# Kernel tuning notes

Hardware: AMD Instinct MI355X
Metric: run time of the kernel (lower is better)

The kernel has to match this reference:

```python
import jax, jax.numpy as jnp
import numpy as np

H, HKV, D, HID = 32, 8, 128, 4096
L, CTX, S = 64, 64, 8192
T = CTX + L
HALF = D // 2
EPS = 1e-6
WP = 4096


def setup_inputs() -> dict:
    key = jax.random.key(0)
    ks = jax.random.split(key, 16)
    f = jnp.float32
    w = 0.02
    return {
        "x": jax.random.normal(ks[0], (1, L, HID), f),
        "x_ctx": jax.random.normal(ks[1], (1, CTX, HID), f),
        "cos_q": jax.random.uniform(ks[2], (1, 1, L, HALF), f, -1.0, 1.0),
        "sin_q": jax.random.uniform(ks[3], (1, 1, L, HALF), f, -1.0, 1.0),
        "cos_k": jax.random.uniform(ks[4], (1, 1, T, HALF), f, -1.0, 1.0),
        "sin_k": jax.random.uniform(ks[5], (1, 1, T, HALF), f, -1.0, 1.0),
        "cache_K_in": jax.random.normal(ks[6], (1, HKV, S, D), f),
        "cache_V_in": jax.random.normal(ks[7], (1, HKV, S, D), f),
        "causal_mask": jnp.ones((1, 1, L, WP + T), dtype=bool),
        "Wq": jax.random.normal(ks[8], (HID, H * D), f) * w,
        "Wk": jax.random.normal(ks[9], (HID, HKV * D), f) * w,
        "Wv": jax.random.normal(ks[10], (HID, HKV * D), f) * w,
        "Wo": jax.random.normal(ks[11], (H * D, HID), f) * w,
        "q_norm_w": jnp.ones((D,), f),
        "k_norm_w": jnp.ones((D,), f),
        "write_pos": WP,
        "rotate": 0,
    }


def _rmsnorm(x, w):
    # normalize over head_dim (last axis)
    var = jnp.mean(x * x, axis=-1, keepdims=True)
    return x * jax.lax.rsqrt(var + EPS) * w


def _rope(x, cos, sin):
    # x: (B, H, T, D); cos/sin: (1, 1, T, HALF) -- rotate-half convention
    x1, x2 = x[..., :HALF], x[..., HALF:]
    return jnp.concatenate([x1 * cos - x2 * sin, x2 * cos + x1 * sin], axis=-1)


def reference(x, x_ctx, cos_q, sin_q, cos_k, sin_k, cache_K_in, cache_V_in,
              causal_mask, Wq, Wk, Wv, Wo, q_norm_w, k_norm_w, write_pos, rotate):
    c = jnp.concatenate([x_ctx, x], axis=1)                  # (1, T, HID)
    q = (x @ Wq).reshape(1, L, H, D)
    k = (c @ Wk).reshape(1, T, HKV, D)
    v = (c @ Wv).reshape(1, T, HKV, D)
    q = _rmsnorm(q, q_norm_w).transpose(0, 2, 1, 3)          # (1, H, L, D)
    k = _rmsnorm(k, k_norm_w).transpose(0, 2, 1, 3)          # (1, HKV, T, D)
    v = v.transpose(0, 2, 1, 3)                               # (1, HKV, T, D)
    q = _rope(q, cos_q, sin_q)
    k = _rope(k, cos_k, sin_k)

    if rotate:  # static Python branch (rotate is a compile-time constant)
        attend_K = jnp.concatenate([cache_K_in[:, :, T:S], k], axis=2)
        attend_V = jnp.concatenate([cache_V_in[:, :, T:S], v], axis=2)
    elif write_pos == 0:
        attend_K, attend_V = k, v
    else:
        attend_K = jnp.concatenate([cache_K_in[:, :, :write_pos], k], axis=2)
        attend_V = jnp.concatenate([cache_V_in[:, :, :write_pos], v], axis=2)

    rep = H // HKV
    scale = jnp.float32(D) ** -0.5
    qg = q.reshape(1, HKV, rep, L, D)
    # grouped attention: broadcast KV heads inline instead of materializing expand
    scores = jnp.einsum('bgrld,bgad->bgrla', qg, attend_K) * scale
    scores = jnp.where(causal_mask[:, :, None], scores, -jnp.inf)  # (1,1,1,L,A) bcast
    probs = jax.nn.softmax(scores, axis=-1)
    o = jnp.einsum('bgrla,bgad->bgrld', probs, attend_V)     # (1, HKV, rep, L, D)
    o = o.reshape(1, H, L, D).transpose(0, 2, 1, 3).reshape(1, L, H * D)
    return (o @ Wo, k, v)
```

## Files before the change

kernel.cpp:

```cpp
#include <hip/hip_runtime.h>

typedef unsigned short u16;
typedef __bf16 bf16x8 __attribute__((ext_vector_type(8)));
typedef float f32x4 __attribute__((ext_vector_type(4)));
typedef u16 u16x8 __attribute__((ext_vector_type(8)));

#define NSPLIT 22
#define KSPLIT 4
#define KC 1024
#define NKT 16
#define OSPLIT 8
#define SCALE_Q 0.08838834764831843f

__device__ __forceinline__ u16 f2bf(float f) {
    unsigned u = __builtin_bit_cast(unsigned, f);
    u += 0x7fff + ((u >> 16) & 1);
    return (u16)(u >> 16);
}
__device__ __forceinline__ float bf2f(u16 h) {
    unsigned u = ((unsigned)h) << 16;
    return __builtin_bit_cast(float, u);
}
__device__ __forceinline__ f32x4 mfma16(bf16x8 a, bf16x8 b, f32x4 c) {
    return __builtin_amdgcn_mfma_f32_16x16x32_bf16(a, b, c, 0, 0, 0);
}

__global__ __launch_bounds__(256)
void k_prep(const float* __restrict__ x, const float* __restrict__ xctx,
            u16* __restrict__ fragA)
{
    int tid = blockIdx.x * 256 + threadIdx.x;
    int row = tid >> 9;
    int kc = tid & 511;
    int k0 = kc << 3;
    const float* src = (row < 64) ? (xctx + (size_t)row * 4096)
                                  : (x + (size_t)(row - 64) * 4096);
    f32x4 v0 = *(const f32x4*)&src[k0];
    f32x4 v1 = *(const f32x4*)&src[k0 + 4];
    u16x8 o;
    o[0] = f2bf(v0[0]); o[1] = f2bf(v0[1]); o[2] = f2bf(v0[2]); o[3] = f2bf(v0[3]);
    o[4] = f2bf(v1[0]); o[5] = f2bf(v1[1]); o[6] = f2bf(v1[2]); o[7] = f2bf(v1[3]);
    int ks32 = k0 >> 5;
    int lg = (k0 >> 3) & 3;
    int rt = row >> 4;
    int l = lg * 16 + (row & 15);
    *(u16x8*)&fragA[(((size_t)ks32 * 8 + rt) * 64 + l) * 8] = o;
}

__global__ __launch_bounds__(256)
void k_qkv(const u16* __restrict__ fragA,
           const float* __restrict__ Wq, const float* __restrict__ Wk,
           const float* __restrict__ Wv, float* __restrict__ part)
{
    const int col0 = blockIdx.x * 32;
    const int ksp = blockIdx.y;
    const int ks0 = ksp * KC;
    const float* W; int ldw, cbase, mat;
    if (col0 < 4096)      { W = Wq; ldw = 4096; cbase = col0;        mat = 0; }
    else if (col0 < 5120) { W = Wk; ldw = 1024; cbase = col0 - 4096; mat = 1; }
    else                  { W = Wv; ldw = 1024; cbase = col0 - 5120; mat = 2; }
    const bool full = (mat != 0);
    const int rowbase = full ? 0 : 64;

    __shared__ __align__(16) u16 Bs[32 * 64];

    const int t = threadIdx.x;
    const int w = t >> 6, l = t & 63;
    const int lm = l & 15, lg = l >> 4;

    const int bk = (t >> 3) << 1;
    const int bn4 = (t & 7) << 2;

    f32x4 pb[2];
    f32x4 acc[2][2] = {};

    const int rt0 = full ? (w * 2) : (4 + w);

    #define QKV_BLOAD(kt_)                                                     \
    {                                                                          \
        const int kg = ks0 + (kt_) * 64;                                       \
        pb[0] = *(const f32x4*)&W[(size_t)(kg + bk) * ldw + cbase + bn4];      \
        pb[1] = *(const f32x4*)&W[(size_t)(kg + bk + 1) * ldw + cbase + bn4];  \
    }

    #define QKV_BSTORE()                                                       \
    {                                                                          \
        _Pragma("unroll")                                                      \
        for (int j = 0; j < 4; j++) {                                          \
            int n = bn4 + j;                                                   \
            int idx = n * 64 + (bk ^ (((n >> 1) & 7) << 3));                   \
            ushort2 v2; v2.x = f2bf(pb[0][j]); v2.y = f2bf(pb[1][j]);          \
            *(ushort2*)&Bs[idx] = v2;                                          \
        }                                                                      \
    }

    QKV_BLOAD(0);
    #pragma unroll 1
    for (int kt = 0; kt < NKT; kt++) {
        if (kt) __syncthreads();
        QKV_BSTORE();
        __syncthreads();
        if (kt + 1 < NKT) QKV_BLOAD(kt + 1);
        const int ks32b = (ks0 >> 5) + kt * 2;
        #pragma unroll
        for (int ks = 0; ks < 2; ks++) {
            const int koff = ks * 32 + lg * 8;
            bf16x8 a0 = *(const bf16x8*)
                &fragA[(((size_t)(ks32b + ks) * 8 + rt0) * 64 + l) * 8];
            bf16x8 bfr[2];
            #pragma unroll
            for (int nt = 0; nt < 2; nt++) {
                int n = nt * 16 + lm;
                bfr[nt] = *(const bf16x8*)&Bs[n * 64 + (koff ^ (((n >> 1) & 7) << 3))];
            }
            acc[0][0] = mfma16(a0, bfr[0], acc[0][0]);
            acc[0][1] = mfma16(a0, bfr[1], acc[0][1]);
            if (full) {
                bf16x8 a1 = *(const bf16x8*)
                    &fragA[(((size_t)(ks32b + ks) * 8 + rt0 + 1) * 64 + l) * 8];
                acc[1][0] = mfma16(a1, bfr[0], acc[1][0]);
                acc[1][1] = mfma16(a1, bfr[1], acc[1][1]);
            }
        }
    }

    const int wrows = full ? 32 : 16;
    const int mts = full ? 2 : 1;
    #pragma unroll
    for (int mt = 0; mt < 2; mt++) {
        if (mt >= mts) break;
        #pragma unroll
        for (int nt = 0; nt < 2; nt++)
            #pragma unroll
            for (int r = 0; r < 4; r++) {
                int grow = rowbase + w * wrows + mt * 16 + lg * 4 + r;
                part[((size_t)ksp * 128 + grow) * 6144 + col0 + nt * 16 + lm] =
                    acc[mt][nt][r];
            }
    }
    #undef QKV_BLOAD
    #undef QKV_BSTORE
}

__global__ __launch_bounds__(256)
void k_normrope(const float* __restrict__ part,
                const float* __restrict__ cosq, const float* __restrict__ sinq,
                const float* __restrict__ cosk, const float* __restrict__ sink,
                const float* __restrict__ qnw, const float* __restrict__ knw,
                u16* __restrict__ qb, u16* __restrict__ kb,
                float* __restrict__ outk, float* __restrict__ outv,
                u16* __restrict__ vbw)
{
    int wid = blockIdx.x * 4 + (threadIdx.x >> 6);
    int lane = threadIdx.x & 63;
    if (wid < 2048) {
        int h = wid >> 6, lq = wid & 63;
        size_t ro = (size_t)(64 + lq) * 6144 + h * 128;
        float x1 = 0.f, x2 = 0.f;
        #pragma unroll
        for (int s = 0; s < KSPLIT; s++) {
            x1 += part[(size_t)s * 786432 + ro + lane];
            x2 += part[(size_t)s * 786432 + ro + lane + 64];
        }
        float ss = x1 * x1 + x2 * x2;
        #pragma unroll
        for (int off = 32; off; off >>= 1) ss += __shfl_xor(ss, off);
        float rms = rsqrtf(ss * (1.0f / 128.0f) + 1e-6f);
        float a = x1 * rms * qnw[lane];
        float b = x2 * rms * qnw[lane + 64];
        float c = cosq[lq * 64 + lane], s = sinq[lq * 64 + lane];
        u16* qo = qb + ((size_t)h * 64 + lq) * 128;
        qo[lane]      = f2bf((a * c - b * s) * SCALE_Q);
        qo[lane + 64] = f2bf((b * c + a * s) * SCALE_Q);
    } else if (wid < 3072) {
        int rr = wid - 2048;
        int kh = rr >> 7, tt = rr & 127;
        size_t ro = (size_t)tt * 6144 + 4096 + kh * 128;
        float x1 = 0.f, x2 = 0.f;
        #pragma unroll
        for (int s = 0; s < KSPLIT; s++) {
            x1 += part[(size_t)s * 786432 + ro + lane];
            x2 += part[(size_t)s * 786432 + ro + lane + 64];
        }
        float ss = x1 * x1 + x2 * x2;
        #pragma unroll
        for (int off = 32; off; off >>= 1) ss += __shfl_xor(ss, off);
        float rms = rsqrtf(ss * (1.0f / 128.0f) + 1e-6f);
        float a = x1 * rms * knw[lane];
        float b = x2 * rms * knw[lane + 64];
        float c = cosk[tt * 64 + lane], s = sink[tt * 64 + lane];
        float o1 = a * c - b * s, o2 = b * c + a * s;
        size_t oi = ((size_t)kh * 128 + tt) * 128;
        outk[oi + lane] = o1; outk[oi + lane + 64] = o2;
        kb[oi + lane] = f2bf(o1); kb[oi + lane + 64] = f2bf(o2);
    } else {
        int rr = wid - 3072;
        int kh = rr >> 7, tt = rr & 127;
        size_t ro = (size_t)tt * 6144 + 5120 + kh * 128;
        float v1 = 0.f, v2 = 0.f;
        #pragma unroll
        for (int s = 0; s < KSPLIT; s++) {
            v1 += part[(size_t)s * 786432 + ro + lane];
            v2 += part[(size_t)s * 786432 + ro + lane + 64];
        }
        size_t oi = ((size_t)kh * 128 + tt) * 128;
        outv[oi + lane] = v1; outv[oi + lane + 64] = v2;
        vbw[oi + lane] = f2bf(v1); vbw[oi + lane + 64] = f2bf(v2);
    }
}

__global__ __launch_bounds__(256)
void k_attn(const u16* __restrict__ qb, const u16* __restrict__ kbw,
            const u16* __restrict__ vbw,
            const float* __restrict__ cacheK, const float* __restrict__ cacheV,
            u16* __restrict__ opart, float* __restrict__ lpart)
{
    const int split = blockIdx.x;
    const int kh = blockIdx.y;
    const int t = threadIdx.x;
    const int w = t >> 6, l = t & 63;
    const int lm = l & 15, lg = l >> 4;

    __shared__ __align__(16) u16 Ks[64][136];
    __shared__ __align__(16) u16 Vs[128][72];
    __shared__ __align__(16) u16 Ps[4][64][40];

    const u16* qh = qb + ((size_t)(kh * 4 + w) * 64) * 128;
    bf16x8 aq[4][4];
    #pragma unroll
    for (int mt = 0; mt < 4; mt++)
        #pragma unroll
        for (int ks = 0; ks < 4; ks++)
            aq[mt][ks] = *(const bf16x8*)&qh[(size_t)(mt * 16 + lm) * 128 + ks * 32 + lg * 8];

    f32x4 accO[4][8] = {};
    float lacc[4][4] = {};
    const size_t khK = (size_t)kh * 8192 * 128;

    for (int kbi = 0; kbi < 3; kbi++) {
        const int key0 = split * 192 + kbi * 64;
        __syncthreads();
        #pragma unroll
        for (int it = 0; it < 8; it++) {
            int fidx = it * 256 + t;
            int row = fidx >> 5;
            int d4 = (fidx & 31) << 2;
            int key = key0 + row;
            if (key < 4096) {
                float4 kv = *(const float4*)&cacheK[khK + (size_t)key * 128 + d4];
                ushort4 sv; sv.x = f2bf(kv.x); sv.y = f2bf(kv.y);
                sv.z = f2bf(kv.z); sv.w = f2bf(kv.w);
                *(ushort4*)&Ks[row][d4] = sv;
                float4 vv = *(const float4*)&cacheV[khK + (size_t)key * 128 + d4];
                Vs[d4 + 0][row] = f2bf(vv.x);
                Vs[d4 + 1][row] = f2bf(vv.y);
                Vs[d4 + 2][row] = f2bf(vv.z);
                Vs[d4 + 3][row] = f2bf(vv.w);
            } else {
                size_t nb = ((size_t)kh * 128 + (key - 4096)) * 128 + d4;
                ushort4 kv = *(const ushort4*)&kbw[nb];
                *(ushort4*)&Ks[row][d4] = kv;
                ushort4 vv = *(const ushort4*)&vbw[nb];
                Vs[d4 + 0][row] = vv.x;
                Vs[d4 + 1][row] = vv.y;
                Vs[d4 + 2][row] = vv.z;
                Vs[d4 + 3][row] = vv.w;
            }
        }
        __syncthreads();

        f32x4 sa[4][4] = {};
        #pragma unroll
        for (int ks = 0; ks < 4; ks++) {
            bf16x8 bk[4];
            #pragma unroll
            for (int nt = 0; nt < 4; nt++)
                bk[nt] = *(const bf16x8*)&Ks[nt * 16 + lm][ks * 32 + lg * 8];
            #pragma unroll
            for (int mt = 0; mt < 4; mt++)
                #pragma unroll
                for (int nt = 0; nt < 4; nt++)
                    sa[mt][nt] = mfma16(aq[mt][ks], bk[nt], sa[mt][nt]);
        }

        #pragma unroll
        for (int half = 0; half < 2; half++) {
            __syncthreads();
            #pragma unroll
            for (int mt = 0; mt < 4; mt++)
                #pragma unroll
                for (int nt2 = 0; nt2 < 2; nt2++)
                    #pragma unroll
                    for (int r = 0; r < 4; r++) {
                        float e = __expf(sa[mt][half * 2 + nt2][r]);
                        lacc[mt][r] += e;
                        Ps[w][mt * 16 + lg * 4 + r][nt2 * 16 + lm] = f2bf(e);
                    }
            __syncthreads();
            bf16x8 pa[4];
            #pragma unroll
            for (int mt = 0; mt < 4; mt++)
                pa[mt] = *(const bf16x8*)&Ps[w][mt * 16 + lm][lg * 8];
            #pragma unroll
            for (int dt = 0; dt < 8; dt++) {
                bf16x8 vb8 = *(const bf16x8*)&Vs[dt * 16 + lm][half * 32 + lg * 8];
                #pragma unroll
                for (int mt = 0; mt < 4; mt++)
                    accO[mt][dt] = mfma16(pa[mt], vb8, accO[mt][dt]);
            }
        }
    }

    #pragma unroll
    for (int mt = 0; mt < 4; mt++)
        #pragma unroll
        for (int r = 0; r < 4; r++) {
            float v = lacc[mt][r];
            v += __shfl_xor(v, 1);
            v += __shfl_xor(v, 2);
            v += __shfl_xor(v, 4);
            v += __shfl_xor(v, 8);
            lacc[mt][r] = v;
        }

    const size_t base = (((size_t)kh * NSPLIT + split) * 4 + w) * 64;
    if (lm == 0) {
        #pragma unroll
        for (int mt = 0; mt < 4; mt++)
            #pragma unroll
            for (int r = 0; r < 4; r++)
                lpart[base + mt * 16 + lg * 4 + r] = lacc[mt][r];
    }
    #pragma unroll
    for (int mt = 0; mt < 4; mt++)
        #pragma unroll
        for (int dt = 0; dt < 8; dt++)
            #pragma unroll
            for (int r = 0; r < 4; r++)
                opart[(base + mt * 16 + lg * 4 + r) * 128 + dt * 16 + lm] =
                    f2bf(accO[mt][dt][r]);
}

__global__ __launch_bounds__(256)
void k_combine(const u16* __restrict__ opart, const float* __restrict__ lpart,
               u16* __restrict__ obf)
{
    int idx = blockIdx.x * 256 + threadIdx.x;
    int lq = idx >> 12;
    int col = idx & 4095;
    int h = col >> 7, d = col & 127;
    int kh = h >> 2, rep = h & 3;
    float os = 0.f, ls = 0.f;
    #pragma unroll 2
    for (int s = 0; s < NSPLIT; s++) {
        size_t b = (((size_t)kh * NSPLIT + s) * 4 + rep) * 64 + lq;
        os += bf2f(opart[b * 128 + d]);
        ls += lpart[b];
    }
    obf[idx] = f2bf(os / ls);
}

__global__ __launch_bounds__(256)
void k_oproj(const u16* __restrict__ obf, const float* __restrict__ Wo,
             float* __restrict__ parto)
{
    const int col0 = blockIdx.x * 32;
    const int osp = blockIdx.y;
    const int ks0 = osp * (4096 / OSPLIT);

    __shared__ __align__(16) u16 As[64][72];
    __shared__ __align__(16) u16 Bs[32 * 64];

    const int t = threadIdx.x;
    const int w = t >> 6, l = t & 63;
    const int lm = l & 15, lg = l >> 4;

    const int arow = t >> 3;
    const int ac8 = (t & 7) << 3;
    const int bk = (t >> 3) << 1;
    const int bn4 = (t & 7) << 2;

    u16x8 pa[2]; f32x4 pb[2];
    f32x4 acc[2] = {};

    #define OP_LOAD(kt_)                                                       \
    {                                                                          \
        const int kg = ks0 + (kt_) * 64;                                       \
        pa[0] = *(const u16x8*)&obf[(size_t)arow * 4096 + kg + ac8];           \
        pa[1] = *(const u16x8*)&obf[(size_t)(arow + 32) * 4096 + kg + ac8];    \
        pb[0] = *(const f32x4*)&Wo[(size_t)(kg + bk) * 4096 + col0 + bn4];     \
        pb[1] = *(const f32x4*)&Wo[(size_t)(kg + bk + 1) * 4096 + col0 + bn4]; \
    }

    #define OP_STORE()                                                         \
    {                                                                          \
        *(u16x8*)&As[arow][ac8] = pa[0];                                       \
        *(u16x8*)&As[arow + 32][ac8] = pa[1];                                  \
        _Pragma("unroll")                                                      \
        for (int j = 0; j < 4; j++) {                                          \
            int n = bn4 + j;                                                   \
            int idx = n * 64 + (bk ^ (((n >> 1) & 7) << 3));                   \
            ushort2 v2; v2.x = f2bf(pb[0][j]); v2.y = f2bf(pb[1][j]);          \
            *(ushort2*)&Bs[idx] = v2;                                          \
        }                                                                      \
    }

    OP_LOAD(0);
    #pragma unroll 1
    for (int kt = 0; kt < 4096 / OSPLIT / 64; kt++) {
        if (kt) __syncthreads();
        OP_STORE();
        __syncthreads();
        if (kt + 1 < 4096 / OSPLIT / 64) OP_LOAD(kt + 1);
        #pragma unroll
        for (int ks = 0; ks < 2; ks++) {
            const int koff = ks * 32 + lg * 8;
            bf16x8 a0 = *(const bf16x8*)&As[w * 16 + lm][koff];
            #pragma unroll
            for (int nt = 0; nt < 2; nt++) {
                int n = nt * 16 + lm;
                bf16x8 b = *(const bf16x8*)&Bs[n * 64 + (koff ^ (((n >> 1) & 7) << 3))];
                acc[nt] = mfma16(a0, b, acc[nt]);
            }
        }
    }
    #pragma unroll
    for (int nt = 0; nt < 2; nt++)
        #pragma unroll
        for (int r = 0; r < 4; r++)
            parto[((size_t)osp * 64 + w * 16 + lg * 4 + r) * 4096 +
                  col0 + nt * 16 + lm] = acc[nt][r];
    #undef OP_LOAD
    #undef OP_STORE
}

__global__ __launch_bounds__(256)
void k_osum(const float* __restrict__ parto, float* __restrict__ out0)
{
    int idx = blockIdx.x * 256 + threadIdx.x;
    float s = 0.f;
    #pragma unroll
    for (int o = 0; o < OSPLIT; o++)
        s += parto[(size_t)o * 262144 + idx];
    out0[idx] = s;
}

extern "C" void kernel_launch(void* const* d_in, const int* in_sizes, int n_in,
                              void* d_out, int out_size, void* d_ws, size_t ws_size,
                              hipStream_t stream)
{
    (void)in_sizes; (void)n_in; (void)out_size; (void)ws_size;
    const float* x      = (const float*)d_in[0];
    const float* xctx   = (const float*)d_in[1];
    const float* cosq   = (const float*)d_in[2];
    const float* sinq   = (const float*)d_in[3];
    const float* cosk   = (const float*)d_in[4];
    const float* sink   = (const float*)d_in[5];
    const float* cacheK = (const float*)d_in[6];
    const float* cacheV = (const float*)d_in[7];
    const float* Wq     = (const float*)d_in[9];
    const float* Wk     = (const float*)d_in[10];
    const float* Wv     = (const float*)d_in[11];
    const float* Wo     = (const float*)d_in[12];
    const float* qnw    = (const float*)d_in[13];
    const float* knw    = (const float*)d_in[14];

    float* out0 = (float*)d_out;
    float* out1 = out0 + 262144;
    float* out2 = out1 + 131072;

    char* ws = (char*)d_ws;
    float* part  = (float*)(ws + 0);
    u16*   opart = (u16*)(ws + 0);
    float* lpart = (float*)(ws + 11534336);
    float* parto = (float*)(ws + 0);
    u16*   fragA = (u16*)(ws + 12582912);
    u16*   qb    = (u16*)(ws + 12582912);
    u16*   kb    = (u16*)(ws + 13107200);
    u16*   vb    = (u16*)(ws + 13369344);
    u16*   obf   = (u16*)(ws + 13631488);

    k_prep<<<256, 256, 0, stream>>>(x, xctx, fragA);
    k_qkv<<<dim3(192, KSPLIT), 256, 0, stream>>>(fragA, Wq, Wk, Wv, part);
    k_normrope<<<1024, 256, 0, stream>>>(part, cosq, sinq, cosk, sink,
                                         qnw, knw, qb, kb, out1, out2, vb);
    k_attn<<<dim3(NSPLIT, 8), 256, 0, stream>>>(qb, kb, vb, cacheK, cacheV,
                                                opart, lpart);
    k_combine<<<1024, 256, 0, stream>>>(opart, lpart, obf);
    k_oproj<<<dim3(128, OSPLIT), 256, 0, stream>>>(obf, Wo, parto);
    k_osum<<<1024, 256, 0, stream>>>(parto, out0);
}
```

Baseline: 94.48 us.

## Template QKV split-K factor, use 8-way split when workspace allows, vectorize combine

```diff
diff --git a/kernel.cpp b/kernel.cpp
--- a/kernel.cpp
+++ b/kernel.cpp
@@ -6,9 +6,6 @@
 typedef u16 u16x8 __attribute__((ext_vector_type(8)));
 
 #define NSPLIT 22
-#define KSPLIT 4
-#define KC 1024
-#define NKT 16
 #define OSPLIT 8
 #define SCALE_Q 0.08838834764831843f
 
@@ -47,14 +44,17 @@
     *(u16x8*)&fragA[(((size_t)ks32 * 8 + rt) * 64 + l) * 8] = o;
 }
 
+template<int KS>
 __global__ __launch_bounds__(256)
 void k_qkv(const u16* __restrict__ fragA,
            const float* __restrict__ Wq, const float* __restrict__ Wk,
            const float* __restrict__ Wv, float* __restrict__ part)
 {
+    constexpr int KCk = 4096 / KS;
+    constexpr int NKTk = KCk / 64;
     const int col0 = blockIdx.x * 32;
     const int ksp = blockIdx.y;
-    const int ks0 = ksp * KC;
+    const int ks0 = ksp * KCk;
     const float* W; int ldw, cbase, mat;
     if (col0 < 4096)      { W = Wq; ldw = 4096; cbase = col0;        mat = 0; }
     else if (col0 < 5120) { W = Wk; ldw = 1024; cbase = col0 - 4096; mat = 1; }
@@ -96,23 +96,23 @@
 
     QKV_BLOAD(0);
     #pragma unroll 1
-    for (int kt = 0; kt < NKT; kt++) {
+    for (int kt = 0; kt < NKTk; kt++) {
         if (kt) __syncthreads();
         QKV_BSTORE();
         __syncthreads();
-        if (kt + 1 < NKT) QKV_BLOAD(kt + 1);
+        if (kt + 1 < NKTk) QKV_BLOAD(kt + 1);
         const int ks32b = (ks0 >> 5) + kt * 2;
         #pragma unroll
         for (int ks = 0; ks < 2; ks++) {
             const int koff = ks * 32 + lg * 8;
-            bf16x8 a0 = *(const bf16x8*)
-                &fragA[(((size_t)(ks32b + ks) * 8 + rt0) * 64 + l) * 8];
             bf16x8 bfr[2];
             #pragma unroll
             for (int nt = 0; nt < 2; nt++) {
                 int n = nt * 16 + lm;
                 bfr[nt] = *(const bf16x8*)&Bs[n * 64 + (koff ^ (((n >> 1) & 7) << 3))];
             }
+            bf16x8 a0 = *(const bf16x8*)
+                &fragA[(((size_t)(ks32b + ks) * 8 + rt0) * 64 + l) * 8];
             acc[0][0] = mfma16(a0, bfr[0], acc[0][0]);
             acc[0][1] = mfma16(a0, bfr[1], acc[0][1]);
             if (full) {
@@ -142,6 +142,7 @@
     #undef QKV_BSTORE
 }
 
+template<int KS>
 __global__ __launch_bounds__(256)
 void k_normrope(const float* __restrict__ part,
                 const float* __restrict__ cosq, const float* __restrict__ sinq,
@@ -158,7 +159,7 @@
         size_t ro = (size_t)(64 + lq) * 6144 + h * 128;
         float x1 = 0.f, x2 = 0.f;
         #pragma unroll
-        for (int s = 0; s < KSPLIT; s++) {
+        for (int s = 0; s < KS; s++) {
             x1 += part[(size_t)s * 786432 + ro + lane];
             x2 += part[(size_t)s * 786432 + ro + lane + 64];
         }
@@ -178,7 +179,7 @@
         size_t ro = (size_t)tt * 6144 + 4096 + kh * 128;
         float x1 = 0.f, x2 = 0.f;
         #pragma unroll
-        for (int s = 0; s < KSPLIT; s++) {
+        for (int s = 0; s < KS; s++) {
             x1 += part[(size_t)s * 786432 + ro + lane];
             x2 += part[(size_t)s * 786432 + ro + lane + 64];
         }
@@ -199,7 +200,7 @@
         size_t ro = (size_t)tt * 6144 + 5120 + kh * 128;
         float v1 = 0.f, v2 = 0.f;
         #pragma unroll
-        for (int s = 0; s < KSPLIT; s++) {
+        for (int s = 0; s < KS; s++) {
             v1 += part[(size_t)s * 786432 + ro + lane];
             v2 += part[(size_t)s * 786432 + ro + lane + 64];
         }
@@ -209,6 +210,7 @@
     }
 }
 
+template<int NSP, int NBLK>
 __global__ __launch_bounds__(256)
 void k_attn(const u16* __restrict__ qb, const u16* __restrict__ kbw,
             const u16* __restrict__ vbw,
@@ -237,8 +239,8 @@
     float lacc[4][4] = {};
     const size_t khK = (size_t)kh * 8192 * 128;
 
-    for (int kbi = 0; kbi < 3; kbi++) {
-        const int key0 = split * 192 + kbi * 64;
+    for (int kbi = 0; kbi < NBLK; kbi++) {
+        const int key0 = split * (64 * NBLK) + kbi * 64;
         __syncthreads();
         #pragma unroll
         for (int it = 0; it < 8; it++) {
@@ -323,7 +325,7 @@
             lacc[mt][r] = v;
         }
 
-    const size_t base = (((size_t)kh * NSPLIT + split) * 4 + w) * 64;
+    const size_t base = (((size_t)kh * NSP + split) * 4 + w) * 64;
     if (lm == 0) {
         #pragma unroll
         for (int mt = 0; mt < 4; mt++)
@@ -341,23 +343,31 @@
                     f2bf(accO[mt][dt][r]);
 }
 
+template<int NSP>
 __global__ __launch_bounds__(256)
 void k_combine(const u16* __restrict__ opart, const float* __restrict__ lpart,
                u16* __restrict__ obf)
 {
     int idx = blockIdx.x * 256 + threadIdx.x;
-    int lq = idx >> 12;
-    int col = idx & 4095;
-    int h = col >> 7, d = col & 127;
+    int lq = idx >> 9;
+    int c8 = (idx & 511) << 3;
+    int h = c8 >> 7, d = c8 & 127;
     int kh = h >> 2, rep = h & 3;
-    float os = 0.f, ls = 0.f;
+    float os[8] = {};
+    float ls = 0.f;
     #pragma unroll 2
-    for (int s = 0; s < NSPLIT; s++) {
-        size_t b = (((size_t)kh * NSPLIT + s) * 4 + rep) * 64 + lq;
-        os += bf2f(opart[b * 128 + d]);
+    for (int s = 0; s < NSP; s++) {
+        size_t b = (((size_t)kh * NSP + s) * 4 + rep) * 64 + lq;
+        u16x8 v = *(const u16x8*)&opart[b * 128 + d];
+        #pragma unroll
+        for (int j = 0; j < 8; j++) os[j] += bf2f(v[j]);
         ls += lpart[b];
     }
-    obf[idx] = f2bf(os / ls);
+    float inv = 1.0f / ls;
+    u16x8 o;
+    #pragma unroll
+    for (int j = 0; j < 8; j++) o[j] = f2bf(os[j] * inv);
+    *(u16x8*)&obf[(size_t)lq * 4096 + c8] = o;
 }
 
 __global__ __launch_bounds__(256)
@@ -449,7 +459,7 @@
                               void* d_out, int out_size, void* d_ws, size_t ws_size,
                               hipStream_t stream)
 {
-    (void)in_sizes; (void)n_in; (void)out_size; (void)ws_size;
+    (void)in_sizes; (void)n_in; (void)out_size;
     const float* x      = (const float*)d_in[0];
     const float* xctx   = (const float*)d_in[1];
     const float* cosq   = (const float*)d_in[2];
@@ -469,24 +479,34 @@
     float* out1 = out0 + 262144;
     float* out2 = out1 + 131072;
 
+    const bool ks8 = (ws_size >= 26738688ull);
     char* ws = (char*)d_ws;
+    const size_t regB = ks8 ? 25165824ull : 12582912ull;
+
     float* part  = (float*)(ws + 0);
     u16*   opart = (u16*)(ws + 0);
     float* lpart = (float*)(ws + 11534336);
     float* parto = (float*)(ws + 0);
-    u16*   fragA = (u16*)(ws + 12582912);
-    u16*   qb    = (u16*)(ws + 12582912);
-    u16*   kb    = (u16*)(ws + 13107200);
-    u16*   vb    = (u16*)(ws + 13369344);
-    u16*   obf   = (u16*)(ws + 13631488);
+    u16*   fragA = (u16*)(ws + regB);
+    u16*   qb    = (u16*)(ws + regB);
+    u16*   kb    = (u16*)(ws + regB + 524288);
+    u16*   vb    = (u16*)(ws + regB + 786432);
+    u16*   obf   = (u16*)(ws + regB + 1048576);
 
     k_prep<<<256, 256, 0, stream>>>(x, xctx, fragA);
-    k_qkv<<<dim3(192, KSPLIT), 256, 0, stream>>>(fragA, Wq, Wk, Wv, part);
-    k_normrope<<<1024, 256, 0, stream>>>(part, cosq, sinq, cosk, sink,
-                                         qnw, knw, qb, kb, out1, out2, vb);
-    k_attn<<<dim3(NSPLIT, 8), 256, 0, stream>>>(qb, kb, vb, cacheK, cacheV,
-                                                opart, lpart);
-    k_combine<<<1024, 256, 0, stream>>>(opart, lpart, obf);
+    if (ks8) {
+        k_qkv<8><<<dim3(192, 8), 256, 0, stream>>>(fragA, Wq, Wk, Wv, part);
+        k_normrope<8><<<1024, 256, 0, stream>>>(part, cosq, sinq, cosk, sink,
+                                                qnw, knw, qb, kb, out1, out2, vb);
+    } else {
+        k_qkv<4><<<dim3(192, 4), 256, 0, stream>>>(fragA, Wq, Wk, Wv, part);
+        k_normrope<4><<<1024, 256, 0, stream>>>(part, cosq, sinq, cosk, sink,
+                                                qnw, knw, qb, kb, out1, out2, vb);
+    }
+    k_attn<NSPLIT, 3><<<dim3(NSPLIT, 8), 256, 0, stream>>>(qb, kb, vb,
+                                                           cacheK, cacheV,
+                                                           opart, lpart);
+    k_combine<NSPLIT><<<128, 256, 0, stream>>>(opart, lpart, obf);
     k_oproj<<<dim3(128, OSPLIT), 256, 0, stream>>>(obf, Wo, parto);
     k_osum<<<1024, 256, 0, stream>>>(parto, out0);
 }
```

Result: faster. 89.55 us (-5.2%).
